# Kernel tuning notes

Measured on AMD Instinct MI355X. Metric: run time of the kernel, lower is better.

## Reference

```python
import jax, jax.numpy as jnp
import numpy as np

D_MODEL = 1024
N_HEAD = 16
D_K = D_MODEL // N_HEAD


def setup_inputs() -> dict:
    key = jax.random.key(0)
    ks = jax.random.split(key, 12)
    B, S = 2, 2048
    s = 1.0 / np.sqrt(D_MODEL)
    return {
        "query": jax.random.normal(ks[0], (B, S, D_MODEL), jnp.float32),
        "key": jax.random.normal(ks[1], (B, S, D_MODEL), jnp.float32),
        "value": jax.random.normal(ks[2], (B, S, D_MODEL), jnp.float32),
        "Wq": jax.random.normal(ks[3], (D_MODEL, D_MODEL), jnp.float32) * s,
        "bq": jnp.zeros((D_MODEL,), jnp.float32),
        "Wk": jax.random.normal(ks[4], (D_MODEL, D_MODEL), jnp.float32) * s,
        "bk": jnp.zeros((D_MODEL,), jnp.float32),
        "Wv": jax.random.normal(ks[5], (D_MODEL, D_MODEL), jnp.float32) * s,
        "bv": jnp.zeros((D_MODEL,), jnp.float32),
        "Wo": jax.random.normal(ks[6], (D_MODEL, D_MODEL), jnp.float32) * s,
        "bo": jnp.zeros((D_MODEL,), jnp.float32),
    }


def reference(query, key, value, Wq, bq, Wk, bk, Wv, bv, Wo, bo):
    B, S, _ = query.shape
    # QKV projections (torch Linear: x @ W.T + b)
    q = query @ Wq.T + bq
    k = key @ Wk.T + bk
    v = value @ Wv.T + bv
    # [B, S, H, Dk] -> [B, H, S, Dk]
    q = q.reshape(B, S, N_HEAD, D_K).transpose(0, 2, 1, 3)
    k = k.reshape(B, -1, N_HEAD, D_K).transpose(0, 2, 1, 3)
    v = v.reshape(B, -1, N_HEAD, D_K).transpose(0, 2, 1, 3)
    # scores [B, H, Sq, Sk]
    attn = jnp.einsum("bhqd,bhkd->bhqk", q, k) / jnp.sqrt(jnp.float32(D_K))
    attn = jax.nn.softmax(attn, axis=-1)  # dropout p=0 -> identity
    out = jnp.einsum("bhqk,bhkd->bhqd", attn, v)
    out = out.transpose(0, 2, 1, 3).reshape(B, S, D_MODEL)
    return out @ Wo.T + bo
```

## Files before the change

### kernel.cpp

```cpp
#include <hip/hip_runtime.h>
#include <cstdint>
#include <cstddef>

#define DM 1024
#define NHEAD 16
#define DKH 64
#define SEQLEN 2048
#define NBATCH 2
#define MTOT (NBATCH * SEQLEN)

typedef __attribute__((ext_vector_type(8))) short bf16x8;
typedef __attribute__((ext_vector_type(4))) float f32x4;
typedef __attribute__((ext_vector_type(16))) float f32x16;
typedef __attribute__((ext_vector_type(2))) unsigned int u32x2;

#define QSCALE 0.18033688011112042f

__device__ __forceinline__ uint16_t f2bf(float f) {
  uint32_t x = __float_as_uint(f);
  uint32_t r = x + 0x7FFFu + ((x >> 16) & 1u);
  return (uint16_t)(r >> 16);
}

__device__ __forceinline__ uint32_t cvtpk(float a, float b) {
  uint32_t r;
  asm("v_cvt_pk_bf16_f32 %0, %1, %2" : "=v"(r) : "v"(a), "v"(b));
  return r;
}

__device__ __forceinline__ float exp2_fast(float x) {
  float r;
  asm("v_exp_f32 %0, %1" : "=v"(r) : "v"(x));
  return r;
}

__device__ __forceinline__ float max3f(float a, float b, float c) {
  float r;
  asm("v_max3_f32 %0, %1, %2, %3" : "=v"(r) : "v"(a), "v"(b), "v"(c));
  return r;
}

__device__ __forceinline__ void gload_lds16(const void* g, void* l) {
  __builtin_amdgcn_global_load_lds(
      (const __attribute__((address_space(1))) void*)g,
      (__attribute__((address_space(3))) void*)l, 16, 0, 0);
}

__device__ __forceinline__ int fsw(int r) { return ((r + (r >> 3)) & 7) << 4; }

struct CvtArgs {
  const float* src[7];
  uint16_t* dst[7];
  int end4[7];
};

__global__ void cvt_all_kernel(CvtArgs a) {
  int i = blockIdx.x * blockDim.x + threadIdx.x;
  int r = 0;
#pragma unroll
  for (int j = 0; j < 7; ++j)
    if (i >= a.end4[j]) r = j + 1;
  if (r >= 7) return;
  int local = i - (r == 0 ? 0 : a.end4[r - 1]);
  float4 v = reinterpret_cast<const float4*>(a.src[r])[local];
  uint64_t p = (uint64_t)f2bf(v.x) | ((uint64_t)f2bf(v.y) << 16) |
               ((uint64_t)f2bf(v.z) << 32) | ((uint64_t)f2bf(v.w) << 48);
  reinterpret_cast<uint64_t*>(a.dst[r])[local] = p;
}

__device__ __forceinline__ void gemm_stage(const uint16_t* __restrict__ A,
                                           const uint16_t* __restrict__ Bt,
                                           int brow, int bcol, int k0,
                                           char* smem, int buf, int wave, int lane) {
#pragma unroll
  for (int t = 0; t < 8; ++t) {
    const int o = t * 4096 + wave * 1024 + lane * 16;
    const uint16_t* g;
    if (t < 4) {
      const int row = o >> 7, kk = (o & 127) >> 1;
      g = A + (size_t)(brow + row) * DM + (k0 + kk);
    } else {
      const int o2 = o - 16384;
      const int row = o2 >> 7, kk = (o2 & 127) >> 1;
      g = Bt + (size_t)(bcol + row) * DM + (k0 + kk);
    }
    gload_lds16(g, smem + buf * 32768 + t * 4096 + wave * 1024);
  }
}

__global__ __launch_bounds__(256)
void gemm_qkv(const uint16_t* __restrict__ xq, const uint16_t* __restrict__ xk,
              const uint16_t* __restrict__ xv, const uint16_t* __restrict__ wqkv,
              const float* __restrict__ bqp, const float* __restrict__ bkp,
              const float* __restrict__ bvp, uint16_t* __restrict__ Qp,
              uint16_t* __restrict__ Kp, uint16_t* __restrict__ VTp) {
  __shared__ uint16_t smem[2 * 2 * 128 * 64];
  const int tid = threadIdx.x;
  const int wave = tid >> 6, lane = tid & 63;
  const int l15 = lane & 15, l4 = lane >> 4;
  const int proj = blockIdx.y >> 3;
  const int brow = blockIdx.x * 128, bcol = (blockIdx.y & 7) * 128;
  const int wr = (wave >> 1) * 64, wc = (wave & 1) * 64;
  const uint16_t* A = proj == 0 ? xq : proj == 1 ? xk : xv;
  const uint16_t* Bt = wqkv + (size_t)proj * DM * DM;
  const float* bias = proj == 0 ? bqp : proj == 1 ? bkp : bvp;

  const f32x4 fzero = {0.f, 0.f, 0.f, 0.f};
  f32x4 acc[4][4];
#pragma unroll
  for (int m = 0; m < 4; ++m)
#pragma unroll
    for (int n = 0; n < 4; ++n) acc[m][n] = fzero;

  gemm_stage(A, Bt, brow, bcol, 0, (char*)smem, 0, wave, lane);
  int cur = 0;
  for (int k0 = 0; k0 < DM; k0 += 64) {
    __syncthreads();
    if (k0 + 64 < DM)
      gemm_stage(A, Bt, brow, bcol, k0 + 64, (char*)smem, cur ^ 1, wave, lane);
    const uint16_t* At = smem + cur * 16384;
    const uint16_t* Bs = At + 8192;
#pragma unroll
    for (int ks = 0; ks < 2; ++ks) {
      bf16x8 a[4], b[4];
#pragma unroll
      for (int m = 0; m < 4; ++m)
        a[m] = *(const bf16x8*)(At + (wr + m * 16 + l15) * 64 + ks * 32 + l4 * 8);
#pragma unroll
      for (int n = 0; n < 4; ++n)
        b[n] = *(const bf16x8*)(Bs + (wc + n * 16 + l15) * 64 + ks * 32 + l4 * 8);
#pragma unroll
      for (int m = 0; m < 4; ++m)
#pragma unroll
        for (int n = 0; n < 4; ++n)
          acc[m][n] = __builtin_amdgcn_mfma_f32_16x16x32_bf16(a[m], b[n], acc[m][n], 0, 0, 0);
    }
    cur ^= 1;
  }

  const float scale = proj == 0 ? QSCALE : 1.0f;
  uint16_t* dstQK = proj == 0 ? Qp : Kp;
#pragma unroll
  for (int m = 0; m < 4; ++m) {
#pragma unroll
    for (int n = 0; n < 4; ++n) {
      const int gcol = bcol + wc + n * 16 + l15;
      const float bv = bias[gcol];
      if (proj == 2) {
        const int grow0 = brow + wr + m * 16 + l4 * 4;
        const int b_ = grow0 >> 11, s_ = grow0 & 2047;
        const int h_ = gcol >> 6, d_ = gcol & 63;
        uint16_t* dst = VTp + ((size_t)((b_ * NHEAD + h_) * DKH + d_)) * SEQLEN + s_;
        uint64_t pk = (uint64_t)f2bf(acc[m][n][0] + bv) |
                      ((uint64_t)f2bf(acc[m][n][1] + bv) << 16) |
                      ((uint64_t)f2bf(acc[m][n][2] + bv) << 32) |
                      ((uint64_t)f2bf(acc[m][n][3] + bv) << 48);
        *(uint64_t*)dst = pk;
      } else {
#pragma unroll
        for (int r = 0; r < 4; ++r) {
          const int grow = brow + wr + m * 16 + l4 * 4 + r;
          dstQK[(size_t)grow * DM + gcol] = f2bf((acc[m][n][r] + bv) * scale);
        }
      }
    }
  }
}

__global__ __launch_bounds__(256)
void gemm_out(const uint16_t* __restrict__ A, const uint16_t* __restrict__ Bt,
              const float* __restrict__ bias, float* __restrict__ C) {
  __shared__ uint16_t smem[2 * 2 * 128 * 64];
  const int tid = threadIdx.x;
  const int wave = tid >> 6, lane = tid & 63;
  const int l15 = lane & 15, l4 = lane >> 4;
  const int brow = blockIdx.x * 128, bcol = blockIdx.y * 128;
  const int wr = (wave >> 1) * 64, wc = (wave & 1) * 64;

  const f32x4 fzero = {0.f, 0.f, 0.f, 0.f};
  f32x4 acc[4][4];
#pragma unroll
  for (int m = 0; m < 4; ++m)
#pragma unroll
    for (int n = 0; n < 4; ++n) acc[m][n] = fzero;

  gemm_stage(A, Bt, brow, bcol, 0, (char*)smem, 0, wave, lane);
  int cur = 0;
  for (int k0 = 0; k0 < DM; k0 += 64) {
    __syncthreads();
    if (k0 + 64 < DM)
      gemm_stage(A, Bt, brow, bcol, k0 + 64, (char*)smem, cur ^ 1, wave, lane);
    const uint16_t* At = smem + cur * 16384;
    const uint16_t* Bs = At + 8192;
#pragma unroll
    for (int ks = 0; ks < 2; ++ks) {
      bf16x8 a[4], b[4];
#pragma unroll
      for (int m = 0; m < 4; ++m)
        a[m] = *(const bf16x8*)(At + (wr + m * 16 + l15) * 64 + ks * 32 + l4 * 8);
#pragma unroll
      for (int n = 0; n < 4; ++n)
        b[n] = *(const bf16x8*)(Bs + (wc + n * 16 + l15) * 64 + ks * 32 + l4 * 8);
#pragma unroll
      for (int m = 0; m < 4; ++m)
#pragma unroll
        for (int n = 0; n < 4; ++n)
          acc[m][n] = __builtin_amdgcn_mfma_f32_16x16x32_bf16(a[m], b[n], acc[m][n], 0, 0, 0);
    }
    cur ^= 1;
  }

#pragma unroll
  for (int m = 0; m < 4; ++m) {
#pragma unroll
    for (int n = 0; n < 4; ++n) {
      const int gcol = bcol + wc + n * 16 + l15;
      const float bv = bias[gcol];
#pragma unroll
      for (int r = 0; r < 4; ++r) {
        const int grow = brow + wr + m * 16 + l4 * 4 + r;
        C[(size_t)grow * DM + gcol] = acc[m][n][r] + bv;
      }
    }
  }
}

__device__ __forceinline__ void stage_kv(const uint16_t* __restrict__ Kg,
                                         const uint16_t* __restrict__ Vg,
                                         char* buf, int wave, int lane) {
#pragma unroll
  for (int i = 0; i < 2; ++i) {
    const int base = i * 4096 + wave * 1024;
    const int row = i * 32 + wave * 8 + (lane >> 3);
    const int esw = (((lane & 7) << 4) ^ fsw(row)) >> 1;
    gload_lds16(Kg + (size_t)row * DM + esw, buf + base);
    gload_lds16(Vg + (size_t)row * SEQLEN + esw, buf + 8192 + base);
  }
}

__global__ __launch_bounds__(256)
void attn_fwd_kernel(const uint16_t* __restrict__ Qp, const uint16_t* __restrict__ Kp,
                     const uint16_t* __restrict__ VTp, uint16_t* __restrict__ Op) {
  __shared__ __align__(16) char lds[32768];
  const int tid = threadIdx.x;
  const int wave = tid >> 6, lane = tid & 63;
  const int l31 = lane & 31, hi = lane >> 5;
  const int bb = blockIdx.z, h = blockIdx.y;
  const int q0 = blockIdx.x * 128;

  const int qrow = q0 + wave * 32 + l31;
  const uint16_t* qb = Qp + ((size_t)(bb * SEQLEN + qrow)) * DM + h * DKH;
  bf16x8 qf[4];
#pragma unroll
  for (int ds = 0; ds < 4; ++ds)
    qf[ds] = *(const bf16x8*)(qb + ds * 16 + hi * 8);

  bf16x8 onesf;
#pragma unroll
  for (int j = 0; j < 8; ++j) onesf[j] = (short)0x3F80;

  f32x16 oacc[2], lacc;
#pragma unroll
  for (int m = 0; m < 2; ++m)
#pragma unroll
    for (int r = 0; r < 16; ++r) oacc[m][r] = 0.f;
#pragma unroll
  for (int r = 0; r < 16; ++r) lacc[r] = 0.f;
  float mrow = -1e30f;

  const uint16_t* Kg = Kp + ((size_t)(bb * SEQLEN)) * DM + h * DKH;
  const uint16_t* Vg = VTp + ((size_t)((bb * NHEAD + h) * DKH)) * SEQLEN;

  stage_kv(Kg, Vg, lds, wave, lane);

  const int NT = SEQLEN / 64;
  for (int t = 0; t < NT; ++t) {
    __syncthreads();
    if (t + 1 < NT)
      stage_kv(Kg + (size_t)(t + 1) * 64 * DM, Vg + (t + 1) * 64,
               lds + ((t + 1) & 1) * 16384, wave, lane);
    const char* kb = lds + (t & 1) * 16384;
    const char* vb = kb + 8192;

    f32x16 sacc[2];
#pragma unroll
    for (int n = 0; n < 2; ++n)
#pragma unroll
      for (int r = 0; r < 16; ++r) sacc[n][r] = 0.f;
    __builtin_amdgcn_s_setprio(1);
#pragma unroll
    for (int n = 0; n < 2; ++n) {
      const int kr = 32 * n + l31;
      const char* krow = kb + kr * 128;
      const int f = fsw(kr);
#pragma unroll
      for (int ds = 0; ds < 4; ++ds) {
        const bf16x8 kf = *(const bf16x8*)(krow + ((ds * 32 + hi * 16) ^ f));
        sacc[n] = __builtin_amdgcn_mfma_f32_32x32x16_bf16(kf, qf[ds], sacc[n], 0, 0, 0);
      }
    }
    __builtin_amdgcn_s_setprio(0);

    float ma = max3f(sacc[0][0], sacc[0][1], sacc[0][2]);
    ma = max3f(ma, sacc[0][3], sacc[0][4]);
    ma = max3f(ma, sacc[0][5], sacc[0][6]);
    ma = max3f(ma, sacc[0][7], sacc[0][8]);
    ma = max3f(ma, sacc[0][9], sacc[0][10]);
    ma = max3f(ma, sacc[0][11], sacc[0][12]);
    ma = max3f(ma, sacc[0][13], sacc[0][14]);
    float mb = max3f(sacc[1][0], sacc[1][1], sacc[1][2]);
    mb = max3f(mb, sacc[1][3], sacc[1][4]);
    mb = max3f(mb, sacc[1][5], sacc[1][6]);
    mb = max3f(mb, sacc[1][7], sacc[1][8]);
    mb = max3f(mb, sacc[1][9], sacc[1][10]);
    mb = max3f(mb, sacc[1][11], sacc[1][12]);
    mb = max3f(mb, sacc[1][13], sacc[1][14]);
    float mx = max3f(fmaxf(ma, sacc[0][15]), mb, sacc[1][15]);
    mx = fmaxf(mx, __shfl_xor(mx, 32, 64));

    float mnew = mrow;
    if (__any(mx > mrow + 8.f)) {
      mnew = fmaxf(mrow, mx);
      const float scl = exp2_fast(mrow - mnew);
#pragma unroll
      for (int m = 0; m < 2; ++m)
#pragma unroll
        for (int r = 0; r < 16; ++r) oacc[m][r] *= scl;
      lacc[0] *= scl;
    }
    mrow = mnew;

#pragma unroll
    for (int n = 0; n < 2; ++n) {
      float pv[16];
#pragma unroll
      for (int r = 0; r < 16; ++r) pv[r] = exp2_fast(sacc[n][r] - mnew);
      const uint32_t c0 = cvtpk(pv[0], pv[1]),   c1 = cvtpk(pv[2], pv[3]);
      const uint32_t c2 = cvtpk(pv[4], pv[5]),   c3 = cvtpk(pv[6], pv[7]);
      const uint32_t c4 = cvtpk(pv[8], pv[9]),   c5 = cvtpk(pv[10], pv[11]);
      const uint32_t c6 = cvtpk(pv[12], pv[13]), c7 = cvtpk(pv[14], pv[15]);
      const u32x2 r02 = __builtin_amdgcn_permlane32_swap(c0, c2, false, false);
      const u32x2 r13 = __builtin_amdgcn_permlane32_swap(c1, c3, false, false);
      const u32x2 r46 = __builtin_amdgcn_permlane32_swap(c4, c6, false, false);
      const u32x2 r57 = __builtin_amdgcn_permlane32_swap(c5, c7, false, false);
      union { uint32_t w[4]; bf16x8 v; } f0, f1;
      f0.w[0] = r02.x; f0.w[1] = r13.x; f0.w[2] = r02.y; f0.w[3] = r13.y;
      f1.w[0] = r46.x; f1.w[1] = r57.x; f1.w[2] = r46.y; f1.w[3] = r57.y;

      __builtin_amdgcn_s_setprio(1);
#pragma unroll
      for (int m = 0; m < 2; ++m) {
        const int vr = 32 * m + l31;
        const char* vrow = vb + vr * 128;
        const int f = fsw(vr);
        const bf16x8 v0 = *(const bf16x8*)(vrow + ((n * 64 + hi * 16) ^ f));
        const bf16x8 v1 = *(const bf16x8*)(vrow + ((n * 64 + 32 + hi * 16) ^ f));
        oacc[m] = __builtin_amdgcn_mfma_f32_32x32x16_bf16(v0, f0.v, oacc[m], 0, 0, 0);
        oacc[m] = __builtin_amdgcn_mfma_f32_32x32x16_bf16(v1, f1.v, oacc[m], 0, 0, 0);
      }
      lacc = __builtin_amdgcn_mfma_f32_32x32x16_bf16(onesf, f0.v, lacc, 0, 0, 0);
      lacc = __builtin_amdgcn_mfma_f32_32x32x16_bf16(onesf, f1.v, lacc, 0, 0, 0);
      __builtin_amdgcn_s_setprio(0);
    }
  }

  const float il = 1.0f / lacc[0];
  uint16_t* ob = Op + ((size_t)(bb * SEQLEN + qrow)) * DM + h * DKH;
#pragma unroll
  for (int m = 0; m < 2; ++m)
#pragma unroll
    for (int rq = 0; rq < 4; ++rq) {
      const uint32_t w0 = cvtpk(oacc[m][4 * rq + 0] * il, oacc[m][4 * rq + 1] * il);
      const uint32_t w1 = cvtpk(oacc[m][4 * rq + 2] * il, oacc[m][4 * rq + 3] * il);
      *(uint64_t*)(ob + 32 * m + 8 * rq + 4 * hi) =
          (uint64_t)w0 | ((uint64_t)w1 << 32);
    }
}

extern "C" void kernel_launch(void* const* d_in, const int* in_sizes, int n_in,
                              void* d_out, int out_size, void* d_ws, size_t ws_size,
                              hipStream_t stream) {
  (void)in_sizes; (void)n_in; (void)out_size; (void)ws_size;
  const float* query = (const float*)d_in[0];
  const float* key_i = (const float*)d_in[1];
  const float* value = (const float*)d_in[2];
  const float* Wq = (const float*)d_in[3];
  const float* bq = (const float*)d_in[4];
  const float* Wk = (const float*)d_in[5];
  const float* bk = (const float*)d_in[6];
  const float* Wv = (const float*)d_in[7];
  const float* bv = (const float*)d_in[8];
  const float* Wo = (const float*)d_in[9];
  const float* bo = (const float*)d_in[10];
  float* out = (float*)d_out;

  char* ws = (char*)d_ws;
  const size_t MB = 1ull << 20;
  uint16_t* xq  = (uint16_t*)(ws + 0 * MB);
  uint16_t* xk  = (uint16_t*)(ws + 8 * MB);
  uint16_t* xv  = (uint16_t*)(ws + 16 * MB);
  uint16_t* wqkv = (uint16_t*)(ws + 24 * MB);
  uint16_t* wob = (uint16_t*)(ws + 30 * MB);
  uint16_t* Qp  = (uint16_t*)(ws + 32 * MB);
  uint16_t* Kp  = (uint16_t*)(ws + 40 * MB);
  uint16_t* VTp = (uint16_t*)(ws + 48 * MB);
  uint16_t* AO  = (uint16_t*)(ws + 56 * MB);

  const int n4x = (MTOT * DM) / 4;
  const int n4w = (DM * DM) / 4;
  CvtArgs ca;
  ca.src[0] = query; ca.dst[0] = xq;
  ca.src[1] = key_i; ca.dst[1] = xk;
  ca.src[2] = value; ca.dst[2] = xv;
  ca.src[3] = Wq;    ca.dst[3] = wqkv;
  ca.src[4] = Wk;    ca.dst[4] = wqkv + DM * DM;
  ca.src[5] = Wv;    ca.dst[5] = wqkv + 2 * DM * DM;
  ca.src[6] = Wo;    ca.dst[6] = wob;
  int acc = 0;
  for (int j = 0; j < 7; ++j) { acc += (j < 3) ? n4x : n4w; ca.end4[j] = acc; }
  const int blk = 256;
  cvt_all_kernel<<<(acc + blk - 1) / blk, blk, 0, stream>>>(ca);

  dim3 gq(MTOT / 128, 24);
  gemm_qkv<<<gq, 256, 0, stream>>>(xq, xk, xv, wqkv, bq, bk, bv, Qp, Kp, VTp);

  dim3 ga(SEQLEN / 128, NHEAD, NBATCH);
  attn_fwd_kernel<<<ga, 256, 0, stream>>>(Qp, Kp, VTp, AO);

  dim3 gg(MTOT / 128, DM / 128);
  gemm_out<<<gg, 256, 0, stream>>>(AO, wob, bo, out);
}
```

Measured before the change: 131.3 us.

## Fuse fp32-to-bf16 activation conversion into QKV GEMM A-tile loading

The QKV GEMM now reads the fp32 query/key/value tensors directly, converting them to bf16 in registers and writing them into LDS, in place of a separate conversion pass that wrote bf16 copies to workspace. This drops a full read/write round trip over three 4096x1024 activation tensors and shrinks the conversion kernel to weights only. In exchange, the GEMM loads twice the A bytes per tile through registers instead of direct global-to-LDS loads, which adds register pressure and VALU work inside the main loop. The attention kernel also seeds the first score MFMA with a zero vector instead of zeroing its accumulators each tile.

```diff
diff --git a/kernel.cpp b/kernel.cpp
--- a/kernel.cpp
+++ b/kernel.cpp
@@ -49,18 +49,18 @@
 __device__ __forceinline__ int fsw(int r) { return ((r + (r >> 3)) & 7) << 4; }
 
 struct CvtArgs {
-  const float* src[7];
-  uint16_t* dst[7];
-  int end4[7];
+  const float* src[4];
+  uint16_t* dst[4];
+  int end4[4];
 };
 
 __global__ void cvt_all_kernel(CvtArgs a) {
   int i = blockIdx.x * blockDim.x + threadIdx.x;
   int r = 0;
 #pragma unroll
-  for (int j = 0; j < 7; ++j)
+  for (int j = 0; j < 4; ++j)
     if (i >= a.end4[j]) r = j + 1;
-  if (r >= 7) return;
+  if (r >= 4) return;
   int local = i - (r == 0 ? 0 : a.end4[r - 1]);
   float4 v = reinterpret_cast<const float4*>(a.src[r])[local];
   uint64_t p = (uint64_t)f2bf(v.x) | ((uint64_t)f2bf(v.y) << 16) |
@@ -68,29 +68,9 @@
   reinterpret_cast<uint64_t*>(a.dst[r])[local] = p;
 }
 
-__device__ __forceinline__ void gemm_stage(const uint16_t* __restrict__ A,
-                                           const uint16_t* __restrict__ Bt,
-                                           int brow, int bcol, int k0,
-                                           char* smem, int buf, int wave, int lane) {
-#pragma unroll
-  for (int t = 0; t < 8; ++t) {
-    const int o = t * 4096 + wave * 1024 + lane * 16;
-    const uint16_t* g;
-    if (t < 4) {
-      const int row = o >> 7, kk = (o & 127) >> 1;
-      g = A + (size_t)(brow + row) * DM + (k0 + kk);
-    } else {
-      const int o2 = o - 16384;
-      const int row = o2 >> 7, kk = (o2 & 127) >> 1;
-      g = Bt + (size_t)(bcol + row) * DM + (k0 + kk);
-    }
-    gload_lds16(g, smem + buf * 32768 + t * 4096 + wave * 1024);
-  }
-}
-
 __global__ __launch_bounds__(256)
-void gemm_qkv(const uint16_t* __restrict__ xq, const uint16_t* __restrict__ xk,
-              const uint16_t* __restrict__ xv, const uint16_t* __restrict__ wqkv,
+void gemm_qkv(const float* __restrict__ xq, const float* __restrict__ xk,
+              const float* __restrict__ xv, const uint16_t* __restrict__ wqkv,
               const float* __restrict__ bqp, const float* __restrict__ bkp,
               const float* __restrict__ bvp, uint16_t* __restrict__ Qp,
               uint16_t* __restrict__ Kp, uint16_t* __restrict__ VTp) {
@@ -101,10 +81,13 @@
   const int proj = blockIdx.y >> 3;
   const int brow = blockIdx.x * 128, bcol = (blockIdx.y & 7) * 128;
   const int wr = (wave >> 1) * 64, wc = (wave & 1) * 64;
-  const uint16_t* A = proj == 0 ? xq : proj == 1 ? xk : xv;
+  const float* A = proj == 0 ? xq : proj == 1 ? xk : xv;
   const uint16_t* Bt = wqkv + (size_t)proj * DM * DM;
   const float* bias = proj == 0 ? bqp : proj == 1 ? bkp : bvp;
 
+  const float* arow = A + (size_t)(brow + (tid >> 1)) * DM + (tid & 1) * 32;
+  const int aldsoff = (tid >> 1) * 128 + (tid & 1) * 64;
+
   const f32x4 fzero = {0.f, 0.f, 0.f, 0.f};
   f32x4 acc[4][4];
 #pragma unroll
@@ -112,12 +95,46 @@
 #pragma unroll
     for (int n = 0; n < 4; ++n) acc[m][n] = fzero;
 
-  gemm_stage(A, Bt, brow, bcol, 0, (char*)smem, 0, wave, lane);
+#pragma unroll
+  for (int t = 0; t < 4; ++t) {
+    const int o = t * 4096 + wave * 1024 + lane * 16;
+    const int row = o >> 7, kk = (o & 127) >> 1;
+    gload_lds16(Bt + (size_t)(bcol + row) * DM + kk,
+                (char*)smem + 16384 + t * 4096 + wave * 1024);
+  }
+  {
+    float4 av[8];
+#pragma unroll
+    for (int j = 0; j < 8; ++j) av[j] = *(const float4*)(arow + j * 4);
+    char* ab = (char*)smem + aldsoff;
+#pragma unroll
+    for (int g = 0; g < 4; ++g) {
+      uint4 w;
+      w.x = cvtpk(av[2 * g].x, av[2 * g].y);
+      w.y = cvtpk(av[2 * g].z, av[2 * g].w);
+      w.z = cvtpk(av[2 * g + 1].x, av[2 * g + 1].y);
+      w.w = cvtpk(av[2 * g + 1].z, av[2 * g + 1].w);
+      *(uint4*)(ab + g * 16) = w;
+    }
+  }
+
   int cur = 0;
   for (int k0 = 0; k0 < DM; k0 += 64) {
     __syncthreads();
-    if (k0 + 64 < DM)
-      gemm_stage(A, Bt, brow, bcol, k0 + 64, (char*)smem, cur ^ 1, wave, lane);
+    const bool hasNext = (k0 + 64 < DM);
+    float4 av[8];
+    if (hasNext) {
+#pragma unroll
+      for (int t = 0; t < 4; ++t) {
+        const int o = t * 4096 + wave * 1024 + lane * 16;
+        const int row = o >> 7, kk = (o & 127) >> 1;
+        gload_lds16(Bt + (size_t)(bcol + row) * DM + (k0 + 64 + kk),
+                    (char*)smem + (cur ^ 1) * 32768 + 16384 + t * 4096 + wave * 1024);
+      }
+#pragma unroll
+      for (int j = 0; j < 8; ++j) av[j] = *(const float4*)(arow + k0 + 64 + j * 4);
+    }
+
     const uint16_t* At = smem + cur * 16384;
     const uint16_t* Bs = At + 8192;
 #pragma unroll
@@ -134,6 +151,19 @@
 #pragma unroll
         for (int n = 0; n < 4; ++n)
           acc[m][n] = __builtin_amdgcn_mfma_f32_16x16x32_bf16(a[m], b[n], acc[m][n], 0, 0, 0);
+    }
+
+    if (hasNext) {
+      char* ab = (char*)smem + (cur ^ 1) * 32768 + aldsoff;
+#pragma unroll
+      for (int g = 0; g < 4; ++g) {
+        uint4 w;
+        w.x = cvtpk(av[2 * g].x, av[2 * g].y);
+        w.y = cvtpk(av[2 * g].z, av[2 * g].w);
+        w.z = cvtpk(av[2 * g + 1].x, av[2 * g + 1].y);
+        w.w = cvtpk(av[2 * g + 1].z, av[2 * g + 1].w);
+        *(uint4*)(ab + g * 16) = w;
+      }
     }
     cur ^= 1;
   }
@@ -167,6 +197,26 @@
   }
 }
 
+__device__ __forceinline__ void gemm_stage(const uint16_t* __restrict__ A,
+                                           const uint16_t* __restrict__ Bt,
+                                           int brow, int bcol, int k0,
+                                           char* smem, int buf, int wave, int lane) {
+#pragma unroll
+  for (int t = 0; t < 8; ++t) {
+    const int o = t * 4096 + wave * 1024 + lane * 16;
+    const uint16_t* g;
+    if (t < 4) {
+      const int row = o >> 7, kk = (o & 127) >> 1;
+      g = A + (size_t)(brow + row) * DM + (k0 + kk);
+    } else {
+      const int o2 = o - 16384;
+      const int row = o2 >> 7, kk = (o2 & 127) >> 1;
+      g = Bt + (size_t)(bcol + row) * DM + (k0 + kk);
+    }
+    gload_lds16(g, smem + buf * 32768 + t * 4096 + wave * 1024);
+  }
+}
+
 __global__ __launch_bounds__(256)
 void gemm_out(const uint16_t* __restrict__ A, const uint16_t* __restrict__ Bt,
               const float* __restrict__ bias, float* __restrict__ C) {
@@ -259,13 +309,11 @@
 #pragma unroll
   for (int j = 0; j < 8; ++j) onesf[j] = (short)0x3F80;
 
-  f32x16 oacc[2], lacc;
-#pragma unroll
-  for (int m = 0; m < 2; ++m)
-#pragma unroll
-    for (int r = 0; r < 16; ++r) oacc[m][r] = 0.f;
-#pragma unroll
-  for (int r = 0; r < 16; ++r) lacc[r] = 0.f;
+  f32x16 oacc[2], lacc, zero16;
+#pragma unroll
+  for (int r = 0; r < 16; ++r) {
+    oacc[0][r] = 0.f; oacc[1][r] = 0.f; lacc[r] = 0.f; zero16[r] = 0.f;
+  }
   float mrow = -1e30f;
 
   const uint16_t* Kg = Kp + ((size_t)(bb * SEQLEN)) * DM + h * DKH;
@@ -283,18 +331,16 @@
     const char* vb = kb + 8192;
 
     f32x16 sacc[2];
-#pragma unroll
-    for (int n = 0; n < 2; ++n)
-#pragma unroll
-      for (int r = 0; r < 16; ++r) sacc[n][r] = 0.f;
     __builtin_amdgcn_s_setprio(1);
 #pragma unroll
     for (int n = 0; n < 2; ++n) {
       const int kr = 32 * n + l31;
       const char* krow = kb + kr * 128;
       const int f = fsw(kr);
-#pragma unroll
-      for (int ds = 0; ds < 4; ++ds) {
+      const bf16x8 kf0 = *(const bf16x8*)(krow + ((hi * 16) ^ f));
+      sacc[n] = __builtin_amdgcn_mfma_f32_32x32x16_bf16(kf0, qf[0], zero16, 0, 0, 0);
+#pragma unroll
+      for (int ds = 1; ds < 4; ++ds) {
         const bf16x8 kf = *(const bf16x8*)(krow + ((ds * 32 + hi * 16) ^ f));
         sacc[n] = __builtin_amdgcn_mfma_f32_32x32x16_bf16(kf, qf[ds], sacc[n], 0, 0, 0);
       }
@@ -396,9 +442,6 @@
 
   char* ws = (char*)d_ws;
   const size_t MB = 1ull << 20;
-  uint16_t* xq  = (uint16_t*)(ws + 0 * MB);
-  uint16_t* xk  = (uint16_t*)(ws + 8 * MB);
-  uint16_t* xv  = (uint16_t*)(ws + 16 * MB);
   uint16_t* wqkv = (uint16_t*)(ws + 24 * MB);
   uint16_t* wob = (uint16_t*)(ws + 30 * MB);
   uint16_t* Qp  = (uint16_t*)(ws + 32 * MB);
@@ -406,23 +449,19 @@
   uint16_t* VTp = (uint16_t*)(ws + 48 * MB);
   uint16_t* AO  = (uint16_t*)(ws + 56 * MB);
 
-  const int n4x = (MTOT * DM) / 4;
   const int n4w = (DM * DM) / 4;
   CvtArgs ca;
-  ca.src[0] = query; ca.dst[0] = xq;
-  ca.src[1] = key_i; ca.dst[1] = xk;
-  ca.src[2] = value; ca.dst[2] = xv;
-  ca.src[3] = Wq;    ca.dst[3] = wqkv;
-  ca.src[4] = Wk;    ca.dst[4] = wqkv + DM * DM;
-  ca.src[5] = Wv;    ca.dst[5] = wqkv + 2 * DM * DM;
-  ca.src[6] = Wo;    ca.dst[6] = wob;
+  ca.src[0] = Wq; ca.dst[0] = wqkv;
+  ca.src[1] = Wk; ca.dst[1] = wqkv + DM * DM;
+  ca.src[2] = Wv; ca.dst[2] = wqkv + 2 * DM * DM;
+  ca.src[3] = Wo; ca.dst[3] = wob;
   int acc = 0;
-  for (int j = 0; j < 7; ++j) { acc += (j < 3) ? n4x : n4w; ca.end4[j] = acc; }
+  for (int j = 0; j < 4; ++j) { acc += n4w; ca.end4[j] = acc; }
   const int blk = 256;
   cvt_all_kernel<<<(acc + blk - 1) / blk, blk, 0, stream>>>(ca);
 
   dim3 gq(MTOT / 128, 24);
-  gemm_qkv<<<gq, 256, 0, stream>>>(xq, xk, xv, wqkv, bq, bk, bv, Qp, Kp, VTp);
+  gemm_qkv<<<gq, 256, 0, stream>>>(query, key_i, value, wqkv, bq, bk, bv, Qp, Kp, VTp);
 
   dim3 ga(SEQLEN / 128, NHEAD, NBATCH);
   attn_fwd_kernel<<<ga, 256, 0, stream>>>(Qp, Kp, VTp, AO);
```

New measurement: 154.6 us. +17.8%, slower.
